# Kernel tuning notes

Hardware: AMD Instinct MI355X
Metric: run time of the kernel (lower is better)

## Reference

```python
import jax, jax.numpy as jnp
import numpy as np

STRIDE = 16.0
CROP_H = 14
CROP_W = 14


def setup_inputs() -> dict:
    key = jax.random.key(0)
    k1, k2, k3, k4, k5 = jax.random.split(key, 5)
    N, C, H, W = 4, 256, 50, 50
    M = 512
    feature_map = jax.random.normal(k1, (N, C, H, W), dtype=jnp.float32)
    # boxes in original-image coords (image ~800x800), x1<x2, y1<y2
    x1 = jax.random.uniform(k2, (M,), minval=0.0, maxval=600.0)
    y1 = jax.random.uniform(k3, (M,), minval=0.0, maxval=600.0)
    bw = jax.random.uniform(k4, (M, 2), minval=16.0, maxval=199.0)
    boxes = jnp.stack([x1, y1, x1 + bw[:, 0], y1 + bw[:, 1]], axis=1).astype(jnp.float32)
    box_idx = jax.random.randint(k5, (M,), 0, N, dtype=jnp.int32)
    return {"feature_map": feature_map, "boxes": boxes, "box_idx": box_idx}


def _roi_align(feature_map, boxes, box_idx):
    # TF-style crop_and_resize: sample a CROP_H x CROP_W bilinear grid per box,
    # zero extrapolation outside the feature map.
    H, W = feature_map.shape[2], feature_map.shape[3]
    b = boxes / STRIDE  # image coords -> feature-map coords
    x1, y1, x2, y2 = b[:, 0], b[:, 1], b[:, 2], b[:, 3]
    iy = jnp.arange(CROP_H, dtype=b.dtype)
    ix = jnp.arange(CROP_W, dtype=b.dtype)
    ys = y1[:, None] + iy[None, :] * (y2 - y1)[:, None] / (CROP_H - 1)  # (M, oH)
    xs = x1[:, None] + ix[None, :] * (x2 - x1)[:, None] / (CROP_W - 1)  # (M, oW)

    def crop_one(bi, ys_m, xs_m):
        fm = feature_map[bi]  # (C, H, W) -- gathered per box
        y0 = jnp.floor(ys_m)
        x0 = jnp.floor(xs_m)
        wy = (ys_m - y0)[None, :, None]            # (1, oH, 1)
        wx = (xs_m - x0)[None, None, :] if False else (xs_m - x0)  # (oW,)
        y0i = jnp.clip(y0.astype(jnp.int32), 0, H - 1)
        y1i = jnp.clip(y0i + 1, 0, H - 1)
        x0i = jnp.clip(x0.astype(jnp.int32), 0, W - 1)
        x1i = jnp.clip(x0i + 1, 0, W - 1)
        # interpolate along W first: (C, H, oW)
        g = fm[:, :, x0i] * (1.0 - wx) + fm[:, :, x1i] * wx
        # then along H: (C, oH, oW)
        out = g[:, y0i, :] * (1.0 - wy) + g[:, y1i, :] * wy
        valid = (((ys_m >= 0) & (ys_m <= H - 1))[:, None]
                 & ((xs_m >= 0) & (xs_m <= W - 1))[None, :])
        return jnp.where(valid[None, :, :], out, 0.0)

    return jax.vmap(crop_one)(box_idx, ys, xs)  # (M, C, oH, oW)


def reference(feature_map, boxes, box_idx):
    return _roi_align(feature_map, boxes, box_idx)
```

## Files before the change

kernel.cpp:

```cpp
#include <hip/hip_runtime.h>


typedef float f32x4 __attribute__((ext_vector_type(4)));

constexpr int C_DIM = 256;
constexpr int H_DIM = 50;
constexpr int W_DIM = 50;
constexpr int CW    = 14;
constexpr int NPOS  = 196;
constexpr int PLANE = H_DIM * W_DIM;
constexpr int WC    = 16;
constexpr int WSZ   = 256;
constexpr int ITEM_CH = 8;
constexpr float INV_STRIDE = 1.0f / 16.0f;
constexpr float INV13 = 1.0f / 13.0f;

struct SC { int bi, yLo, xW; float x1, y1, sx, sy; };
struct WT { int w00[4]; float wx[4], ox[4], wy[4], oy[4]; };

__device__ __forceinline__ SC mk_sc(const float* boxes, const int* bidx, int m) {
    float4 bx = reinterpret_cast<const float4*>(boxes)[m];
    SC s;
    s.bi = bidx[m];
    s.x1 = bx.x * INV_STRIDE;
    s.y1 = bx.y * INV_STRIDE;
    s.sx = (bx.z * INV_STRIDE - s.x1) * INV13;
    s.sy = (bx.w * INV_STRIDE - s.y1) * INV13;
    int xLo = min(max((int)floorf(s.x1), 0), W_DIM - 1);
    s.yLo = min(max((int)floorf(s.y1), 0), H_DIM - 1);
    s.xW  = min(xLo, W_DIM - WC);
    return s;
}

__device__ __forceinline__ void mk_wt(const SC& s, int q, WT& W) {
    #pragma unroll
    for (int e = 0; e < 4; ++e) {
        int p  = 4 * q + e;
        int iy = p / CW;
        int ix = p - iy * CW;
        float ys = s.y1 + (float)iy * s.sy;
        float xs = s.x1 + (float)ix * s.sx;
        float y0f = floorf(ys);
        float x0f = floorf(xs);
        float wy = ys - y0f;
        float wx = xs - x0f;
        int y0i = min(max((int)y0f, 0), H_DIM - 1);
        int x0i = min(max((int)x0f, 0), W_DIM - 1);
        bool v = (ys >= 0.0f) && (ys <= (float)(H_DIM - 1)) &&
                 (xs >= 0.0f) && (xs <= (float)(W_DIM - 1));
        W.w00[e] = (y0i - s.yLo) * WC + (x0i - s.xW);
        W.wx[e] = v ? wx : 0.0f;
        W.ox[e] = v ? (1.0f - wx) : 0.0f;
        W.wy[e] = wy; W.oy[e] = 1.0f - wy;
    }
}

__device__ __forceinline__ void stage(const float* fm, const SC& s, int cb,
                                      int wv, int l, float* buf) {
    int row  = l >> 2;
    int quad = l & 3;
    int gy   = min(s.yLo + row, H_DIM - 1);
    const float* g0 = fm + ((size_t)(s.bi * C_DIM + cb + wv * 2)) * PLANE
                         + gy * W_DIM + s.xW + quad * 4;
    float* l0 = &buf[(wv * 2) * WSZ];
    __builtin_amdgcn_global_load_lds(
        (const __attribute__((address_space(1))) unsigned int*)g0,
        (__attribute__((address_space(3))) unsigned int*)l0, 16, 0, 0);
    __builtin_amdgcn_global_load_lds(
        (const __attribute__((address_space(1))) unsigned int*)(g0 + PLANE),
        (__attribute__((address_space(3))) unsigned int*)(l0 + WSZ), 16, 0, 0);
}

__device__ __forceinline__ void comp(const float* buf, const WT& W, float* out,
                                     int m, int cb, int wv, int q) {
    const float* wp = &buf[(wv * 2) * WSZ];
    float* op = out + ((size_t)m * C_DIM + cb + wv * 2) * NPOS + 4 * q;
    #pragma unroll
    for (int k = 0; k < 2; ++k) {
        float rv[4];
        #pragma unroll
        for (int e = 0; e < 4; ++e) {
            float f00 = wp[W.w00[e]];
            float f01 = wp[W.w00[e] + 1];
            float f10 = wp[W.w00[e] + WC];
            float f11 = wp[W.w00[e] + WC + 1];
            float top = f00 * W.ox[e] + f01 * W.wx[e];
            float bot = f10 * W.ox[e] + f11 * W.wx[e];
            rv[e] = top * W.oy[e] + bot * W.wy[e];
        }
        f32x4 r;
        r.x = rv[0]; r.y = rv[1]; r.z = rv[2]; r.w = rv[3];
        *reinterpret_cast<f32x4*>(op) = r;
        wp += WSZ;
        op += NPOS;
    }
}

__global__ __launch_bounds__(256) void roi_align_v17(
    const float* __restrict__ fm,
    const float* __restrict__ boxes,
    const int*   __restrict__ box_idx,
    float*       __restrict__ out)
{
    __shared__ float B0[ITEM_CH * WSZ];
    __shared__ float B1[ITEM_CH * WSZ];

    int bid  = blockIdx.x;
    int xcd  = bid & 7;
    int bxl  = bid >> 3;
    int cb_x = xcd * 32;
    int m0   = 2 * bxl;
    int m1   = m0 + 1;

    int t  = threadIdx.x;
    int wv = t >> 6;
    int l  = t & 63;
    int qq = min(l, 48);

    SC s0 = mk_sc(boxes, box_idx, m0);
    SC s1 = mk_sc(boxes, box_idx, m1);
    asm volatile("" :: "v"(s1.bi), "v"(s1.yLo), "v"(s1.xW),
                       "v"(s1.x1), "v"(s1.y1), "v"(s1.sx), "v"(s1.sy));

    WT W0, W1;
    mk_wt(s0, qq, W0);
    mk_wt(s1, qq, W1);

    stage(fm, s0, cb_x + 0 * ITEM_CH, wv, l, B0);
    stage(fm, s0, cb_x + 1 * ITEM_CH, wv, l, B1);

    #pragma unroll
    for (int j = 0; j < 8; ++j) {
        float* bc = (j & 1) ? B1 : B0;
        int mcur  = (j < 4) ? m0 : m1;
        int cb    = cb_x + (j & 3) * ITEM_CH;

        if (j == 0) {
            asm volatile("s_waitcnt vmcnt(2)" ::: "memory");
        } else {
            asm volatile("s_waitcnt vmcnt(4)" ::: "memory");
        }

        if (l < 49) {
            if (j < 4) comp(bc, W0, out, mcur, cb, wv, l);
            else       comp(bc, W1, out, mcur, cb, wv, l);
        }

        if (j < 6) {
            int jn = j + 2;
            stage(fm, (jn < 4) ? s0 : s1, cb_x + (jn & 3) * ITEM_CH, wv, l, bc);
        }
    }
}

extern "C" void kernel_launch(void* const* d_in, const int* in_sizes, int n_in,
                              void* d_out, int out_size, void* d_ws, size_t ws_size,
                              hipStream_t stream) {
    const float* fm      = (const float*)d_in[0];
    const float* boxes   = (const float*)d_in[1];
    const int*   box_idx = (const int*)d_in[2];
    float* out = (float*)d_out;

    dim3 block(256);
    dim3 grid(2048);
    hipLaunchKernelGGL(roi_align_v17, grid, block, 0, stream,
                       fm, boxes, box_idx, out);
}
```

Baseline: 29.86 us.

## Split warps into producer/compute and store roles with LDS result staging

The kernel is restructured so each block handles one box instead of two, with 384 threads. Four wavefronts stage feature tiles and compute bilinear results into a double-buffered LDS result buffer. Two extra wavefronts write those results to global memory with nontemporal stores, one stage behind, separated by block barriers. The aim is to overlap output stores with loads and compute, but it adds barriers, extra LDS traffic and roughly double the number of blocks.

```diff
diff --git a/kernel.cpp b/kernel.cpp
--- a/kernel.cpp
+++ b/kernel.cpp
@@ -11,7 +11,6 @@
 constexpr int PLANE = H_DIM * W_DIM;
 constexpr int WC    = 16;
 constexpr int WSZ   = 256;
-constexpr int ITEM_CH = 8;
 constexpr float INV_STRIDE = 1.0f / 16.0f;
 constexpr float INV13 = 1.0f / 13.0f;
 
@@ -55,101 +54,97 @@
     }
 }
 
-__device__ __forceinline__ void stage(const float* fm, const SC& s, int cb,
-                                      int wv, int l, float* buf) {
+__device__ __forceinline__ void stageP(const float* fm, const SC& s, int gch,
+                                       int l, float* wbuf) {
     int row  = l >> 2;
     int quad = l & 3;
     int gy   = min(s.yLo + row, H_DIM - 1);
-    const float* g0 = fm + ((size_t)(s.bi * C_DIM + cb + wv * 2)) * PLANE
+    const float* g0 = fm + ((size_t)(s.bi * C_DIM + gch)) * PLANE
                          + gy * W_DIM + s.xW + quad * 4;
-    float* l0 = &buf[(wv * 2) * WSZ];
     __builtin_amdgcn_global_load_lds(
         (const __attribute__((address_space(1))) unsigned int*)g0,
-        (__attribute__((address_space(3))) unsigned int*)l0, 16, 0, 0);
+        (__attribute__((address_space(3))) unsigned int*)wbuf, 16, 0, 0);
     __builtin_amdgcn_global_load_lds(
         (const __attribute__((address_space(1))) unsigned int*)(g0 + PLANE),
-        (__attribute__((address_space(3))) unsigned int*)(l0 + WSZ), 16, 0, 0);
+        (__attribute__((address_space(3))) unsigned int*)(wbuf + WSZ), 16, 0, 0);
 }
 
-__device__ __forceinline__ void comp(const float* buf, const WT& W, float* out,
-                                     int m, int cb, int wv, int q) {
-    const float* wp = &buf[(wv * 2) * WSZ];
-    float* op = out + ((size_t)m * C_DIM + cb + wv * 2) * NPOS + 4 * q;
-    #pragma unroll
-    for (int k = 0; k < 2; ++k) {
-        float rv[4];
-        #pragma unroll
-        for (int e = 0; e < 4; ++e) {
-            float f00 = wp[W.w00[e]];
-            float f01 = wp[W.w00[e] + 1];
-            float f10 = wp[W.w00[e] + WC];
-            float f11 = wp[W.w00[e] + WC + 1];
-            float top = f00 * W.ox[e] + f01 * W.wx[e];
-            float bot = f10 * W.ox[e] + f11 * W.wx[e];
-            rv[e] = top * W.oy[e] + bot * W.wy[e];
-        }
-        f32x4 r;
-        r.x = rv[0]; r.y = rv[1]; r.z = rv[2]; r.w = rv[3];
-        *reinterpret_cast<f32x4*>(op) = r;
-        wp += WSZ;
-        op += NPOS;
-    }
-}
-
-__global__ __launch_bounds__(256) void roi_align_v17(
+__global__ __launch_bounds__(384) void roi_align_v18(
     const float* __restrict__ fm,
     const float* __restrict__ boxes,
     const int*   __restrict__ box_idx,
     float*       __restrict__ out)
 {
-    __shared__ float B0[ITEM_CH * WSZ];
-    __shared__ float B1[ITEM_CH * WSZ];
+    __shared__ float WBuf[4][2][2 * WSZ];
+    __shared__ float RBuf[2][8 * NPOS];
 
     int bid  = blockIdx.x;
     int xcd  = bid & 7;
-    int bxl  = bid >> 3;
+    int m    = bid >> 3;
     int cb_x = xcd * 32;
-    int m0   = 2 * bxl;
-    int m1   = m0 + 1;
 
     int t  = threadIdx.x;
     int wv = t >> 6;
     int l  = t & 63;
-    int qq = min(l, 48);
 
-    SC s0 = mk_sc(boxes, box_idx, m0);
-    SC s1 = mk_sc(boxes, box_idx, m1);
-    asm volatile("" :: "v"(s1.bi), "v"(s1.yLo), "v"(s1.xW),
-                       "v"(s1.x1), "v"(s1.y1), "v"(s1.sx), "v"(s1.sy));
-
-    WT W0, W1;
-    mk_wt(s0, qq, W0);
-    mk_wt(s1, qq, W1);
-
-    stage(fm, s0, cb_x + 0 * ITEM_CH, wv, l, B0);
-    stage(fm, s0, cb_x + 1 * ITEM_CH, wv, l, B1);
+    SC s = mk_sc(boxes, box_idx, m);
+    WT W;
+    if (wv < 4) {
+        mk_wt(s, min(l, 48), W);
+        stageP(fm, s, cb_x + 0 * 8 + wv * 2, l, &WBuf[wv][0][0]);
+    }
 
     #pragma unroll
-    for (int j = 0; j < 8; ++j) {
-        float* bc = (j & 1) ? B1 : B0;
-        int mcur  = (j < 4) ? m0 : m1;
-        int cb    = cb_x + (j & 3) * ITEM_CH;
+    for (int j = 0; j <= 4; ++j) {
+        if (wv < 4 && j < 4) {
+            if (j < 3)
+                stageP(fm, s, cb_x + (j + 1) * 8 + wv * 2, l,
+                       &WBuf[wv][(j + 1) & 1][0]);
+            if (j < 3) asm volatile("s_waitcnt vmcnt(2)" ::: "memory");
+            else       asm volatile("s_waitcnt vmcnt(0)" ::: "memory");
 
-        if (j == 0) {
-            asm volatile("s_waitcnt vmcnt(2)" ::: "memory");
-        } else {
-            asm volatile("s_waitcnt vmcnt(4)" ::: "memory");
+            if (l < 49) {
+                #pragma unroll
+                for (int k = 0; k < 2; ++k) {
+                    const float* wp = &WBuf[wv][j & 1][k * WSZ];
+                    float rv[4];
+                    #pragma unroll
+                    for (int e = 0; e < 4; ++e) {
+                        float f00 = wp[W.w00[e]];
+                        float f01 = wp[W.w00[e] + 1];
+                        float f10 = wp[W.w00[e] + WC];
+                        float f11 = wp[W.w00[e] + WC + 1];
+                        float top = f00 * W.ox[e] + f01 * W.wx[e];
+                        float bot = f10 * W.ox[e] + f11 * W.wx[e];
+                        rv[e] = top * W.oy[e] + bot * W.wy[e];
+                    }
+                    f32x4 r;
+                    r.x = rv[0]; r.y = rv[1]; r.z = rv[2]; r.w = rv[3];
+                    *reinterpret_cast<f32x4*>(
+                        &RBuf[j & 1][(wv * 2 + k) * NPOS + l * 4]) = r;
+                }
+            }
+            asm volatile("s_waitcnt lgkmcnt(0)" ::: "memory");
         }
 
-        if (l < 49) {
-            if (j < 4) comp(bc, W0, out, mcur, cb, wv, l);
-            else       comp(bc, W1, out, mcur, cb, wv, l);
+        if (wv >= 4 && j >= 1) {
+            int b = (j - 1) & 1;
+            if (l < 49) {
+                #pragma unroll
+                for (int k = 0; k < 4; ++k) {
+                    int ch = (wv - 4) * 4 + k;
+                    f32x4 v = *reinterpret_cast<const f32x4*>(
+                        &RBuf[b][ch * NPOS + l * 4]);
+                    float* op = out + ((size_t)(m * C_DIM + cb_x + (j - 1) * 8
+                                                + ch)) * NPOS + l * 4;
+                    __builtin_nontemporal_store(v, reinterpret_cast<f32x4*>(op));
+                }
+            }
         }
 
-        if (j < 6) {
-            int jn = j + 2;
-            stage(fm, (jn < 4) ? s0 : s1, cb_x + (jn & 3) * ITEM_CH, wv, l, bc);
-        }
+        asm volatile("" ::: "memory");
+        __builtin_amdgcn_s_barrier();
+        asm volatile("" ::: "memory");
     }
 }
 
@@ -161,8 +156,8 @@
     const int*   box_idx = (const int*)d_in[2];
     float* out = (float*)d_out;
 
-    dim3 block(256);
-    dim3 grid(2048);
-    hipLaunchKernelGGL(roi_align_v17, grid, block, 0, stream,
+    dim3 block(384);
+    dim3 grid(512 * 8);
+    hipLaunchKernelGGL(roi_align_v18, grid, block, 0, stream,
                        fm, boxes, box_idx, out);
 }
```

After: 33.35 us. 11.7% more time.
